# Kernel tuning notes

Measured on AMD Instinct MI355X. Metric: run time of the kernel, lower is better.

The kernel has to match this reference:

```python
import jax, jax.numpy as jnp
import numpy as np

K_CHUNK = 512  # key-chunk size used by the module when n > 5000


def setup_inputs() -> dict:
    key = jax.random.key(0)
    ks = jax.random.split(key, 9)
    b, n, d = 1, 8192, 512
    s = 1.0 / np.sqrt(d)
    x = jax.random.normal(ks[0], (b, n, d), dtype=jnp.float32)
    Wq = jax.random.normal(ks[1], (d, d), dtype=jnp.float32) * s
    bq = jax.random.normal(ks[2], (d,), dtype=jnp.float32) * 0.01
    Wk = jax.random.normal(ks[3], (d, d), dtype=jnp.float32) * s
    bk = jax.random.normal(ks[4], (d,), dtype=jnp.float32) * 0.01
    Wv = jax.random.normal(ks[5], (d, d), dtype=jnp.float32) * s
    bv = jax.random.normal(ks[6], (d,), dtype=jnp.float32) * 0.01
    Wo = jax.random.normal(ks[7], (d, d), dtype=jnp.float32) * s
    bo = jax.random.normal(ks[8], (d,), dtype=jnp.float32) * 0.01
    return {"x": x, "Wq": Wq, "bq": bq, "Wk": Wk, "bk": bk,
            "Wv": Wv, "bv": bv, "Wo": Wo, "bo": bo}


def reference(x, Wq, bq, Wk, bk, Wv, bv, Wo, bo):
    # Faithful to the n > 5000 branch of SimpleAttenLayer (eval mode: dropout = identity).
    # The q-chunking in the original does not change the math (each q row is independent),
    # so we vectorize over all queries. The k-chunking DOES change the math: softmax is
    # applied within each 512-wide key block, then a second softmax over the concatenated
    # per-block weights, then matmul with full v.
    b, n, d = x.shape
    assert n % K_CHUNK == 0
    q = x @ Wq + bq
    k = x @ Wk + bk
    v = x @ Wv + bv
    scores = jnp.einsum('bnd,bmd->bnm', q, k) / jnp.sqrt(jnp.float32(d))
    # softmax within each key chunk of size K_CHUNK
    w1 = jax.nn.softmax(scores.reshape(b, n, n // K_CHUNK, K_CHUNK), axis=-1)
    w1 = w1.reshape(b, n, n)
    # second (global) softmax over the concatenated chunk weights
    w2 = jax.nn.softmax(w1, axis=-1)
    attn_out = jnp.einsum('bnm,bmd->bnd', w2, v)
    cls_attn_weights = w2[:, 0:1, :]  # [b, 1, n]
    out = x + (attn_out @ Wo + bo)
    return (out, cls_attn_weights)
```

## Files before the change

### kernel.cpp

```cpp
#include <hip/hip_runtime.h>
#include <stdint.h>

typedef unsigned short u16;
typedef uint8_t u8;
typedef __bf16 bf16x8 __attribute__((ext_vector_type(8)));
typedef float f32x4 __attribute__((ext_vector_type(4)));
typedef float f32x16 __attribute__((ext_vector_type(16)));
typedef long i64x2 __attribute__((ext_vector_type(2)));
typedef int i32x8 __attribute__((ext_vector_type(8)));

#define NTOK 8192
#define DD 512
#define CHK 512
#define NCH 16
#define KSPLIT 2
#define KLEN 4096
#define LOG2E 1.4426950408889634f
#define SCL 0.044194173824159216f
#define SCLL 0.063762069130835270f

__device__ __forceinline__ u16 f2bf(float f) {
  union { float f; uint32_t u; } v; v.f = f;
  uint32_t r = v.u + 0x7FFFu + ((v.u >> 16) & 1u);
  return (u16)(r >> 16);
}

template <int CTRL>
__device__ __forceinline__ float dppadd(float x) {
  int y = __builtin_amdgcn_update_dpp(0, __float_as_int(x), CTRL, 0xF, 0xF, true);
  return x + __int_as_float(y);
}
__device__ __forceinline__ float rowsum16(float x) {
  x = dppadd<0xB1>(x);
  x = dppadd<0x4E>(x);
  x = dppadd<0x141>(x);
  x = dppadd<0x140>(x);
  return x;
}

typedef const __attribute__((address_space(1))) unsigned int* gas_t;
typedef __attribute__((address_space(3))) unsigned int* las_t;
__device__ __forceinline__ void gload16(const void* g, void* l) {
  __builtin_amdgcn_global_load_lds((gas_t)g, (las_t)l, 16, 0, 0);
}

__device__ __forceinline__ void vm4bar() {
  asm volatile("s_waitcnt vmcnt(4)\n\ts_barrier" ::: "memory");
}
__device__ __forceinline__ void vm0bar() {
  asm volatile("s_waitcnt vmcnt(0)\n\ts_barrier" ::: "memory");
}
__device__ __forceinline__ void barx() {
  asm volatile("s_barrier" ::: "memory");
}
__device__ __forceinline__ void lgkm0() {
  asm volatile("s_waitcnt lgkmcnt(0)" ::: "memory");
  __builtin_amdgcn_sched_barrier(0);
}

__device__ __forceinline__ int ilv64(int p) {
  const int g = p >> 3;
  return (((g & 3) * 2) + (g >> 2)) * 8 + (p & 7);
}

__global__ void prep_kernel(const float* __restrict__ x, const float* __restrict__ Wq,
                            const float* __restrict__ Wk, const float* __restrict__ Wv,
                            const float* __restrict__ Wo, const float* __restrict__ bq,
                            u16* __restrict__ xb, u16* __restrict__ Wall, u16* __restrict__ WoT,
                            float* __restrict__ lsum, float* __restrict__ q0g) {
  __shared__ float t[32][33];
  const int bid = blockIdx.x;
  const int tid = threadIdx.x;
  if (bid < 4096) {
    int i = bid * 256 + tid;
    if (bid < 32) lsum[bid * 256 + tid] = 0.f;
    float4 v = ((const float4*)x)[i];
    ushort4 o;
    o.x = f2bf(v.x); o.y = f2bf(v.y); o.z = f2bf(v.z); o.w = f2bf(v.w);
    ((ushort4*)xb)[i] = o;
  } else if (bid < 5120) {
    const int tt = bid - 4096;
    const int z = tt >> 8, idx = tt & 255;
    const float* W; u16* WT;
    if (z == 0)      { W = Wq; WT = Wall; }
    else if (z == 1) { W = Wk; WT = Wall + 512 * 512; }
    else if (z == 2) { W = Wv; WT = Wall + 2 * 512 * 512; }
    else             { W = Wo; WT = WoT; }
    const int n0 = (idx & 15) * 32, k0 = (idx >> 4) * 32;
    const int tx = tid & 31, ty = tid >> 5;
    #pragma unroll
    for (int i = 0; i < 4; i++)
      t[ty + 8 * i][tx] = W[(k0 + ty + 8 * i) * DD + n0 + tx];
    __syncthreads();
    #pragma unroll
    for (int i = 0; i < 4; i++)
      WT[(n0 + ty + 8 * i) * DD + k0 + tx] = f2bf(t[tx][ty + 8 * i]);
  } else {
    const int c = (bid - 5120) * 256 + tid;
    float acc = bq[c];
    #pragma unroll 8
    for (int i = 0; i < 512; i++) acc += x[i] * Wq[i * 512 + c];
    q0g[c] = acc;
  }
}

__launch_bounds__(256, 3)
__global__ void qkv_kernel(const u16* __restrict__ A, const u16* __restrict__ Wall,
                           const float* __restrict__ bq, const float* __restrict__ bk,
                           const float* __restrict__ bv, u8* __restrict__ qb8,
                           u8* __restrict__ kb8, u8* __restrict__ vT8) {
  __shared__ __align__(16) u16 As[2][128 * 32];
  __shared__ __align__(16) u16 Bs[2][128 * 32];
  const int m0 = blockIdx.x * 128;
  const int n0g = blockIdx.y * 128;
  const int which = blockIdx.y >> 2;
  const int n0 = n0g & 511;
  const int tid = threadIdx.x;
  const int w = tid >> 6, lane = tid & 63, lm = lane & 15, quad = lane >> 4;
  const int wm = w & 1, wn = w >> 1;
  f32x4 acc[4][4] = {};
  const int soff = tid * 16;
  const int srow = soff >> 6;
  const int scol = soff & 63;
  const char* Ag = (const char*)A + ((size_t)(m0 + srow) * DD) * 2 + scol;
  const char* Bg = (const char*)Wall + ((size_t)(n0g + srow) * DD) * 2 + scol;
  char* Al = (char*)As + w * 1024;
  char* Bl = (char*)Bs + w * 1024;
  const size_t rs = (size_t)64 * DD * 2;

  auto stage = [&](int kk, int buf) {
    const char* ag = Ag + (size_t)kk * 2;
    const char* bg = Bg + (size_t)kk * 2;
    char* al = Al + buf * 8192;
    char* bl = Bl + buf * 8192;
    gload16(ag, al);
    gload16(ag + rs, al + 4096);
    gload16(bg, bl);
    gload16(bg + rs, bl + 4096);
  };

  stage(0, 0);
  for (int t = 0; t < 16; ++t) {
    const int cur = t & 1;
    if (t < 15) { stage((t + 1) * 32, cur ^ 1); vm4bar(); }
    else vm0bar();
    bf16x8 af[4], bfr[4];
    #pragma unroll
    for (int i = 0; i < 4; i++) af[i] = *(const bf16x8*)&As[cur][(wm * 64 + i * 16 + lm) * 32 + quad * 8];
    #pragma unroll
    for (int j = 0; j < 4; j++) bfr[j] = *(const bf16x8*)&Bs[cur][(wn * 64 + j * 16 + lm) * 32 + quad * 8];
    lgkm0();
    #pragma unroll
    for (int i = 0; i < 4; i++)
      #pragma unroll
      for (int j = 0; j < 4; j++)
        acc[i][j] = __builtin_amdgcn_mfma_f32_16x16x32_bf16(af[i], bfr[j], acc[i][j], 0, 0, 0);
    barx();
  }
  const float* bias = (which == 0) ? bq : (which == 1) ? bk : bv;
  u8* tile = (u8*)As;
  #pragma unroll
  for (int i = 0; i < 4; i++) {
    const int rl0 = wm * 64 + i * 16 + quad * 4;
    #pragma unroll
    for (int j = 0; j < 4; j++) {
      const int cl = wn * 64 + j * 16 + lm;
      const float bv_ = bias[n0 + cl];
      if (which == 2) {
        #pragma unroll
        for (int r = 0; r < 4; r++) {
          const float val = acc[i][j][r] + bv_;
          uint32_t pk = __builtin_amdgcn_cvt_pk_fp8_f32(val, val, 0, false);
          const int rl = rl0 + r;
          const int t6 = rl & 63;
          const int tl = (rl & 64) | ((t6 & 15) * 4 + (t6 >> 4));
          tile[cl * 128 + tl] = (u8)(pk & 0xFF);
        }
      } else {
        const int icl = (cl & 64) | ilv64(cl & 63);
        #pragma unroll
        for (int r = 0; r < 4; r++) {
          const float val = acc[i][j][r] + bv_;
          uint32_t pk = __builtin_amdgcn_cvt_pk_fp8_f32(val, val, 0, false);
          tile[(rl0 + r) * 128 + icl] = (u8)(pk & 0xFF);
        }
      }
    }
  }
  __syncthreads();
  const int lrow = tid >> 1, half = tid & 1;
  const uint4* s4 = (const uint4*)(tile + lrow * 128 + half * 64);
  if (which == 2) {
    uint4* p = (uint4*)(vT8 + (size_t)(n0 + lrow) * NTOK + m0 + half * 64);
    #pragma unroll
    for (int k = 0; k < 4; k++) p[k] = s4[k];
  } else {
    u8* dst = (which == 0) ? qb8 : kb8;
    uint4* p = (uint4*)(dst + (size_t)(m0 + lrow) * DD + n0 + half * 64);
    #pragma unroll
    for (int k = 0; k < 4; k++) p[k] = s4[k];
  }
}

__launch_bounds__(256, 3)
__global__ void outproj_kernel(const u16* __restrict__ A, const u16* __restrict__ BT,
                               const float* __restrict__ bias, float* __restrict__ outp,
                               const float* __restrict__ resid) {
  __shared__ __align__(16) u16 As[2][128 * 32];
  __shared__ __align__(16) u16 Bs[2][128 * 32];
  const int m0 = blockIdx.x * 128, n0 = blockIdx.y * 128;
  const int tid = threadIdx.x;
  const int w = tid >> 6, lane = tid & 63, lm = lane & 15, quad = lane >> 4;
  const int wm = w & 1, wn = w >> 1;
  f32x4 acc[4][4] = {};
  const int soff = tid * 16;
  const int srow = soff >> 6;
  const int scol = soff & 63;
  const char* Ag = (const char*)A + ((size_t)(m0 + srow) * DD) * 2 + scol;
  const char* Bg = (const char*)BT + ((size_t)(n0 + srow) * DD) * 2 + scol;
  char* Al = (char*)As + w * 1024;
  char* Bl = (char*)Bs + w * 1024;
  const size_t rs = (size_t)64 * DD * 2;

  auto stage = [&](int kk, int buf) {
    const char* ag = Ag + (size_t)kk * 2;
    const char* bg = Bg + (size_t)kk * 2;
    char* al = Al + buf * 8192;
    char* bl = Bl + buf * 8192;
    gload16(ag, al);
    gload16(ag + rs, al + 4096);
    gload16(bg, bl);
    gload16(bg + rs, bl + 4096);
  };

  stage(0, 0);
  for (int t = 0; t < 16; ++t) {
    const int cur = t & 1;
    if (t < 15) { stage((t + 1) * 32, cur ^ 1); vm4bar(); }
    else vm0bar();
    bf16x8 af[4], bfr[4];
    #pragma unroll
    for (int i = 0; i < 4; i++) af[i] = *(const bf16x8*)&As[cur][(wm * 64 + i * 16 + lm) * 32 + quad * 8];
    #pragma unroll
    for (int j = 0; j < 4; j++) bfr[j] = *(const bf16x8*)&Bs[cur][(wn * 64 + j * 16 + lm) * 32 + quad * 8];
    lgkm0();
    #pragma unroll
    for (int i = 0; i < 4; i++)
      #pragma unroll
      for (int j = 0; j < 4; j++)
        acc[i][j] = __builtin_amdgcn_mfma_f32_16x16x32_bf16(af[i], bfr[j], acc[i][j], 0, 0, 0);
    barx();
  }
  #pragma unroll
  for (int i = 0; i < 4; i++) {
    const int row0 = m0 + wm * 64 + i * 16 + quad * 4;
    #pragma unroll
    for (int j = 0; j < 4; j++) {
      const int col = n0 + wn * 64 + j * 16 + lm;
      const float bv = bias[col];
      #pragma unroll
      for (int r = 0; r < 4; r++) {
        const size_t idx = (size_t)(row0 + r) * DD + col;
        outp[idx] = acc[i][j][r] + bv + resid[idx];
      }
    }
  }
}

template <int MODE>
__launch_bounds__(256, 3)
__global__ void gemm_pv_kernel(const u8* __restrict__ A, const u8* __restrict__ BT,
                               int K, void* __restrict__ outp,
                               const float* __restrict__ lsum) {
  __shared__ __align__(16) u8 As[2][128 * 64];
  __shared__ __align__(16) u8 Bs[2][128 * 64];
  const int m0 = blockIdx.x * 128, n0 = blockIdx.y * 128;
  const int tid = threadIdx.x;
  const int w = tid >> 6, lane = tid & 63;
  const int l31 = lane & 31, kh = lane >> 5;
  const int wm = w & 1, wn = w >> 1;
  f32x16 acc[2][2] = {};
  const int srow = tid >> 2;
  const int scol = ((tid & 3) ^ ((srow >> 1) & 3)) * 16;
  const size_t kbase = (size_t)blockIdx.z * (size_t)K;
  const u8* Ag = A + (size_t)(m0 + srow) * NTOK + kbase + scol;
  const u8* Bg = BT + (size_t)(n0 + srow) * NTOK + kbase + scol;
  u8* Al = (u8*)As + w * 1024;
  u8* Bl = (u8*)Bs + w * 1024;
  const size_t rs = (size_t)64 * NTOK;
  const int s_ = (l31 >> 1) & 3;
  const int c0 = ((kh * 2) ^ s_) * 16;
  const int c1 = ((kh * 2 + 1) ^ s_) * 16;

  auto stage = [&](int kk, int buf) {
    gload16(Ag + kk, Al + buf * 8192);
    gload16(Ag + kk + rs, Al + buf * 8192 + 4096);
    gload16(Bg + kk, Bl + buf * 8192);
    gload16(Bg + kk + rs, Bl + buf * 8192 + 4096);
  };

  stage(0, 0);
  int cur = 0;
  for (int kk = 0; kk < K; kk += 64) {
    if (kk + 64 < K) { stage(kk + 64, cur ^ 1); vm4bar(); }
    else vm0bar();
    i32x8 av[2], bv[2];
    #pragma unroll
    for (int g = 0; g < 2; g++) {
      const int ar = wm * 64 + g * 32 + l31;
      union { i32x8 v; struct { i64x2 lo; i64x2 hi; } p; } ua;
      ua.p.lo = *(const i64x2*)&As[cur][ar * 64 + c0];
      ua.p.hi = *(const i64x2*)&As[cur][ar * 64 + c1];
      av[g] = ua.v;
      const int br = wn * 64 + g * 32 + l31;
      union { i32x8 v; struct { i64x2 lo; i64x2 hi; } p; } ub;
      ub.p.lo = *(const i64x2*)&Bs[cur][br * 64 + c0];
      ub.p.hi = *(const i64x2*)&Bs[cur][br * 64 + c1];
      bv[g] = ub.v;
    }
    lgkm0();
    #pragma unroll
    for (int i = 0; i < 2; i++)
      #pragma unroll
      for (int j = 0; j < 2; j++)
        acc[i][j] = __builtin_amdgcn_mfma_scale_f32_32x32x64_f8f6f4(
            av[i], bv[j], acc[i][j], 0, 0, 0, 0x7F7F7F7F, 0, 0x7F7F7F7F);
    barx();
    cur ^= 1;
  }
  #pragma unroll
  for (int i = 0; i < 2; i++) {
    #pragma unroll
    for (int j = 0; j < 2; j++) {
      #pragma unroll
      for (int r = 0; r < 16; r++) {
        const int row = m0 + wm * 64 + i * 32 + (r & 3) + 8 * (r >> 2) + 4 * kh;
        const int col = n0 + wn * 64 + j * 32 + l31;
        if (MODE == 3) {
          ((u16*)outp)[(size_t)row * DD + col] = f2bf(acc[i][j][r] * (1.0f / lsum[row]));
        } else {
          float* po = (float*)outp + (size_t)blockIdx.z * NTOK * DD;
          po[(size_t)row * DD + col] = acc[i][j][r];
        }
      }
    }
  }
}

__global__ void pv_reduce_kernel(const float* __restrict__ part, const float* __restrict__ lsum,
                                 u16* __restrict__ attnb) {
  const int idx = blockIdx.x * 256 + threadIdx.x;
  const int row = idx >> 7;
  const int c4 = (idx & 127) << 2;
  const float* p = part + (size_t)row * DD + c4;
  const size_t stride = (size_t)NTOK * DD;
  float4 a = *(const float4*)(p);
  float4 b = *(const float4*)(p + stride);
  const float inv = 1.0f / lsum[row];
  ushort4 o;
  o.x = f2bf((a.x + b.x) * inv);
  o.y = f2bf((a.y + b.y) * inv);
  o.z = f2bf((a.z + b.z) * inv);
  o.w = f2bf((a.w + b.w) * inv);
  *(ushort4*)(attnb + (size_t)row * DD + c4) = o;
}

__launch_bounds__(512, 4)
__global__ void scores_kernel(const u8* __restrict__ qb8, const u8* __restrict__ kb8,
                              u8* __restrict__ P8, float* __restrict__ lsum) {
  __shared__ __align__(16) u8 As[2][64 * 64];
  __shared__ __align__(16) u8 Bs[2][512 * 64];
  __shared__ float hS[8][64], hP[8][64], hZ[64];
  const int m0 = blockIdx.x * 64;
  const int c = blockIdx.y;
  const int tid = threadIdx.x;
  const int w = tid >> 6, lane = tid & 63, lm = lane & 15, quad = lane >> 4;
  const int wsl = w;
  f32x4 s[4][4] = {};
  const int srA = tid >> 2;
  const int scS = ((tid & 3) ^ ((srA >> 1) & 3)) * 16;
  const u8* Qg = qb8 + (size_t)(m0 + srA) * DD + scS;
  const u8* Kg = kb8 + (size_t)(c * CHK + srA) * DD + scS;
  u8* Al = (u8*)As + w * 1024;
  u8* Bl = (u8*)Bs + w * 1024;
  const int csel = ((quad ^ ((lm >> 1) & 3)) * 16);

  auto stage = [&](int kk, int buf) {
    u8* al = Al + buf * 4096;
    u8* bl = Bl + buf * 32768;
    if (tid < 256) gload16(Qg + kk, al);
    gload16(Kg + kk, bl);
    gload16(Kg + kk + (size_t)128 * DD, bl + 8192);
    gload16(Kg + kk + (size_t)256 * DD, bl + 16384);
    gload16(Kg + kk + (size_t)384 * DD, bl + 24576);
  };

  stage(0, 0);
  vm0bar();
  #pragma unroll
  for (int t = 0; t < 8; ++t) {
    const int cur = t & 1;
    if (t < 7) stage((t + 1) * 64, cur ^ 1);
    i64x2 afv[4], bfv[4];
    #pragma unroll
    for (int i = 0; i < 4; i++)
      afv[i] = *(const i64x2*)&As[cur][(i * 16 + lm) * 64 + csel];
    #pragma unroll
    for (int j = 0; j < 4; j++)
      bfv[j] = *(const i64x2*)&Bs[cur][(wsl * 64 + j * 16 + lm) * 64 + csel];
    lgkm0();
    __builtin_amdgcn_s_setprio(1);
    #pragma unroll
    for (int i = 0; i < 4; i++)
      #pragma unroll
      for (int j = 0; j < 4; j++) {
        s[i][j] = __builtin_amdgcn_mfma_f32_16x16x32_fp8_fp8(afv[i].x, bfv[j].x, s[i][j], 0, 0, 0);
        s[i][j] = __builtin_amdgcn_mfma_f32_16x16x32_fp8_fp8(afv[i].y, bfv[j].y, s[i][j], 0, 0, 0);
      }
    __builtin_amdgcn_s_setprio(0);
    vm0bar();
  }
  #pragma unroll
  for (int i = 0; i < 4; i++) {
    #pragma unroll
    for (int reg = 0; reg < 4; reg++) {
      float z = 0.f;
      #pragma unroll
      for (int j = 0; j < 4; j++) {
        float e = exp2f(s[i][j][reg] * SCLL);
        s[i][j][reg] = e;
        z += e;
      }
      z = rowsum16(z);
      if (lm == 0) hS[wsl][i * 16 + quad * 4 + reg] = z;
    }
  }
  __syncthreads();
  if (tid < 64) {
    float t = 0.f;
    #pragma unroll
    for (int w2 = 0; w2 < 8; w2++) t += hS[w2][tid];
    hZ[tid] = LOG2E / t;
  }
  __syncthreads();
  const int pbyte = wsl * 64 + lm * 4;
  #pragma unroll
  for (int i = 0; i < 4; i++) {
    #pragma unroll
    for (int reg = 0; reg < 4; reg++) {
      const int rl = i * 16 + quad * 4 + reg;
      const float iz = hZ[rl];
      const float p0 = exp2f(s[i][0][reg] * iz);
      const float p1 = exp2f(s[i][1][reg] * iz);
      const float p2 = exp2f(s[i][2][reg] * iz);
      const float p3 = exp2f(s[i][3][reg] * iz);
      float zp = (p0 + p1) + (p2 + p3);
      zp = rowsum16(zp);
      if (lm == 0) hP[wsl][rl] = zp;
      uint32_t o = __builtin_amdgcn_cvt_pk_fp8_f32(p0, p1, 0, false);
      o = __builtin_amdgcn_cvt_pk_fp8_f32(p2, p3, o, true);
      *(uint32_t*)(P8 + (size_t)(m0 + rl) * NTOK + c * CHK + pbyte) = o;
    }
  }
  __syncthreads();
  if (tid < 64) {
    float t = 0.f;
    #pragma unroll
    for (int w2 = 0; w2 < 8; w2++) t += hP[w2][tid];
    atomicAdd(&lsum[m0 + tid], t);
  }
}

__global__ void cls_u_kernel(const float* __restrict__ Wk, const float* __restrict__ bk,
                             const float* __restrict__ q0g, float* __restrict__ uc) {
  __shared__ float q0[512];
  const int tid = threadIdx.x;
  q0[tid] = q0g[tid];
  q0[tid + 256] = q0g[tid + 256];
  __syncthreads();
  if (blockIdx.x < 8) {
    const int c = blockIdx.x * 64 + (tid >> 2), ii = tid & 3;
    float acc = 0.f;
    #pragma unroll 8
    for (int j = ii; j < 512; j += 4) acc += Wk[(size_t)c * 512 + j] * q0[j];
    acc += __shfl_xor(acc, 1, 64);
    acc += __shfl_xor(acc, 2, 64);
    if (ii == 0) uc[c] = acc;
  } else if (tid < 64) {
    float acc = 0.f;
    #pragma unroll 8
    for (int j = tid; j < 512; j += 64) acc += bk[j] * q0[j];
    #pragma unroll
    for (int off = 1; off < 64; off <<= 1) acc += __shfl_xor(acc, off, 64);
    if (tid == 0) uc[512] = acc;
  }
}

__global__ void cls_scores_kernel(const float* __restrict__ x, const float* __restrict__ uc,
                                  float* __restrict__ s0) {
  __shared__ float u[512];
  __shared__ float c0s;
  int tid = threadIdx.x;
  for (int i = tid; i < 512; i += 256) u[i] = uc[i];
  if (tid == 0) c0s = uc[512];
  __syncthreads();
  int rowg = blockIdx.x * 32 + (tid >> 3);
  int ii = tid & 7;
  const float* xr = x + rowg * 512;
  float acc = 0.f;
  for (int i = ii; i < 512; i += 8) acc += xr[i] * u[i];
  acc += __shfl_xor(acc, 1, 64);
  acc += __shfl_xor(acc, 2, 64);
  acc += __shfl_xor(acc, 4, 64);
  if (ii == 0) s0[rowg] = (acc + c0s) * SCL;
}

__global__ void cls_softmax_kernel(const float* __restrict__ s0, float* __restrict__ out) {
  int tid = threadIdx.x;
  int w = tid >> 6, lane = tid & 63;
  const float* sc = s0 + w * 512;
  float v[8];
  float m = -1e30f;
  #pragma unroll
  for (int j = 0; j < 8; j++) { v[j] = sc[lane * 8 + j]; m = fmaxf(m, v[j]); }
  for (int off = 1; off < 64; off <<= 1) m = fmaxf(m, __shfl_xor(m, off, 64));
  float z = 0.f;
  #pragma unroll
  for (int j = 0; j < 8; j++) { v[j] = expf(v[j] - m); z += v[j]; }
  for (int off = 1; off < 64; off <<= 1) z += __shfl_xor(z, off, 64);
  float invz = 1.f / z;
  float l = 0.f;
  #pragma unroll
  for (int j = 0; j < 8; j++) { v[j] = expf(v[j] * invz); l += v[j]; }
  for (int off = 1; off < 64; off <<= 1) l += __shfl_xor(l, off, 64);
  __shared__ float lw[16];
  if (lane == 0) lw[w] = l;
  __syncthreads();
  float L = 0.f;
  for (int i = 0; i < 16; i++) L += lw[i];
  float invL = 1.f / L;
  #pragma unroll
  for (int j = 0; j < 8; j++) out[w * 512 + lane * 8 + j] = v[j] * invL;
}

extern "C" void kernel_launch(void* const* d_in, const int* in_sizes, int n_in,
                              void* d_out, int out_size, void* d_ws, size_t ws_size,
                              hipStream_t stream) {
  const float* x  = (const float*)d_in[0];
  const float* Wq = (const float*)d_in[1];
  const float* bq = (const float*)d_in[2];
  const float* Wk = (const float*)d_in[3];
  const float* bk = (const float*)d_in[4];
  const float* Wv = (const float*)d_in[5];
  const float* bv = (const float*)d_in[6];
  const float* Wo = (const float*)d_in[7];
  const float* bo = (const float*)d_in[8];
  float* out = (float*)d_out;

  char* ws = (char*)d_ws;
  u16* xb    = (u16*)(ws);
  u16* Wall  = (u16*)(ws + 8388608);
  u16* WoT   = (u16*)(ws + 9961472);
  u8*  qb8   = (u8*)(ws + 10485760);
  u8*  kb8   = (u8*)(ws + 14680064);
  u8*  vT8   = (u8*)(ws + 18874368);
  u16* attnb = (u16*)(ws + 23068672);
  float* q0g = (float*)(ws + 31457280);
  float* uc  = (float*)(ws + 31461376);
  float* s0  = (float*)(ws + 31465472);
  float* lsum= (float*)(ws + 31498240);
  u8*  P8    = (u8*)(ws + 31531008);
  float* part= (float*)(ws + 98639872);
  const size_t need_full = 98639872ULL + (size_t)KSPLIT * NTOK * DD * 4ULL;

  prep_kernel<<<5122, 256, 0, stream>>>(x, Wq, Wk, Wv, Wo, bq, xb, Wall, WoT, lsum, q0g);

  qkv_kernel<<<dim3(NTOK / 128, 12), 256, 0, stream>>>(xb, Wall, bq, bk, bv, qb8, kb8, vT8);

  scores_kernel<<<dim3(NTOK / 64, NCH), 512, 0, stream>>>(qb8, kb8, P8, lsum);

  if (ws_size >= need_full) {
    gemm_pv_kernel<4><<<dim3(NTOK / 128, DD / 128, KSPLIT), 256, 0, stream>>>(
        P8, vT8, KLEN, part, nullptr);
    pv_reduce_kernel<<<NTOK * DD / 4 / 256, 256, 0, stream>>>(part, lsum, attnb);
  } else {
    gemm_pv_kernel<3><<<dim3(NTOK / 128, DD / 128), 256, 0, stream>>>(
        P8, vT8, NTOK, attnb, lsum);
  }

  outproj_kernel<<<dim3(NTOK / 128, DD / 128), 256, 0, stream>>>(attnb, WoT, bo, out, x);

  cls_u_kernel<<<9, 256, 0, stream>>>(Wk, bk, q0g, uc);
  cls_scores_kernel<<<NTOK / 32, 256, 0, stream>>>(x, uc, s0);
  cls_softmax_kernel<<<1, 1024, 0, stream>>>(s0, out + (size_t)NTOK * DD);
}
```

Measured before the change: 300.4 us.

## Fold CLS-row kernels into qkv and outproj launches with ticket-based final softmax

The three small CLS-attention kernels are removed. The u-vector computation becomes an extra grid row of the QKV GEMM launch, and the per-row CLS scores become extra blocks of the output-projection launch. An atomic ticket, reset in the prep kernel, lets the last finishing block run the CLS double softmax. This removes three kernel launches and their serialization tails, at the cost of threadfence/atomic synchronization and extra non-GEMM blocks sharing the GEMM grids.

```diff
diff --git a/kernel.cpp b/kernel.cpp
--- a/kernel.cpp
+++ b/kernel.cpp
@@ -67,13 +67,15 @@
                             const float* __restrict__ Wk, const float* __restrict__ Wv,
                             const float* __restrict__ Wo, const float* __restrict__ bq,
                             u16* __restrict__ xb, u16* __restrict__ Wall, u16* __restrict__ WoT,
-                            float* __restrict__ lsum, float* __restrict__ q0g) {
+                            float* __restrict__ lsum, float* __restrict__ q0g,
+                            unsigned int* __restrict__ ticket) {
   __shared__ float t[32][33];
   const int bid = blockIdx.x;
   const int tid = threadIdx.x;
   if (bid < 4096) {
     int i = bid * 256 + tid;
     if (bid < 32) lsum[bid * 256 + tid] = 0.f;
+    if (bid == 0 && tid == 0) *ticket = 0u;
     float4 v = ((const float4*)x)[i];
     ushort4 o;
     o.x = f2bf(v.x); o.y = f2bf(v.y); o.z = f2bf(v.z); o.w = f2bf(v.w);
@@ -108,14 +110,40 @@
 __global__ void qkv_kernel(const u16* __restrict__ A, const u16* __restrict__ Wall,
                            const float* __restrict__ bq, const float* __restrict__ bk,
                            const float* __restrict__ bv, u8* __restrict__ qb8,
-                           u8* __restrict__ kb8, u8* __restrict__ vT8) {
+                           u8* __restrict__ kb8, u8* __restrict__ vT8,
+                           const float* __restrict__ WkF, const float* __restrict__ bkF,
+                           const float* __restrict__ q0g, float* __restrict__ uc) {
   __shared__ __align__(16) u16 As[2][128 * 32];
   __shared__ __align__(16) u16 Bs[2][128 * 32];
+  const int tid = threadIdx.x;
+  if (blockIdx.y == 12) {
+    if (blockIdx.x >= 9) return;
+    float* q0 = (float*)As;
+    q0[tid] = q0g[tid];
+    q0[tid + 256] = q0g[tid + 256];
+    __syncthreads();
+    if (blockIdx.x < 8) {
+      const int c = blockIdx.x * 64 + (tid >> 2), ii = tid & 3;
+      float acc = 0.f;
+      #pragma unroll 8
+      for (int j = ii; j < 512; j += 4) acc += WkF[(size_t)c * 512 + j] * q0[j];
+      acc += __shfl_xor(acc, 1, 64);
+      acc += __shfl_xor(acc, 2, 64);
+      if (ii == 0) uc[c] = acc;
+    } else if (tid < 64) {
+      float acc = 0.f;
+      #pragma unroll 8
+      for (int j = tid; j < 512; j += 64) acc += bkF[j] * q0[j];
+      #pragma unroll
+      for (int off = 1; off < 64; off <<= 1) acc += __shfl_xor(acc, off, 64);
+      if (tid == 0) uc[512] = acc;
+    }
+    return;
+  }
   const int m0 = blockIdx.x * 128;
   const int n0g = blockIdx.y * 128;
   const int which = blockIdx.y >> 2;
   const int n0 = n0g & 511;
-  const int tid = threadIdx.x;
   const int w = tid >> 6, lane = tid & 63, lm = lane & 15, quad = lane >> 4;
   const int wm = w & 1, wn = w >> 1;
   f32x4 acc[4][4] = {};
@@ -205,11 +233,71 @@
 __launch_bounds__(256, 3)
 __global__ void outproj_kernel(const u16* __restrict__ A, const u16* __restrict__ BT,
                                const float* __restrict__ bias, float* __restrict__ outp,
-                               const float* __restrict__ resid) {
+                               const float* __restrict__ resid, const float* __restrict__ uc,
+                               float* __restrict__ s0, unsigned int* __restrict__ ticket) {
   __shared__ __align__(16) u16 As[2][128 * 32];
   __shared__ __align__(16) u16 Bs[2][128 * 32];
+  const int tid = threadIdx.x;
+  if (blockIdx.y >= 4) {
+    const int cb = (blockIdx.y - 4) * 64 + blockIdx.x;
+    __shared__ float u[512];
+    __shared__ float c0s;
+    __shared__ int sOld;
+    for (int i = tid; i < 512; i += 256) u[i] = uc[i];
+    if (tid == 0) c0s = uc[512];
+    __syncthreads();
+    const int rowg = cb * 32 + (tid >> 3);
+    const int ii = tid & 7;
+    const float* xr = resid + (size_t)rowg * 512;
+    float a2 = 0.f;
+    for (int i = ii; i < 512; i += 8) a2 += xr[i] * u[i];
+    a2 += __shfl_xor(a2, 1, 64);
+    a2 += __shfl_xor(a2, 2, 64);
+    a2 += __shfl_xor(a2, 4, 64);
+    if (ii == 0) s0[rowg] = (a2 + c0s) * SCL;
+    __threadfence();
+    __syncthreads();
+    if (tid == 0) sOld = (int)atomicAdd(ticket, 1u);
+    __syncthreads();
+    if (sOld == 255) {
+      __threadfence();
+      __shared__ float lw2[16];
+      const int wv = tid >> 6, lane = tid & 63;
+      float vv[4][8];
+      #pragma unroll
+      for (int cc = 0; cc < 4; cc++) {
+        const int ch = wv * 4 + cc;
+        const float* sc = s0 + ch * 512;
+        float m = -1e30f;
+        #pragma unroll
+        for (int j = 0; j < 8; j++) { vv[cc][j] = sc[lane * 8 + j]; m = fmaxf(m, vv[cc][j]); }
+        for (int off = 1; off < 64; off <<= 1) m = fmaxf(m, __shfl_xor(m, off, 64));
+        float z = 0.f;
+        #pragma unroll
+        for (int j = 0; j < 8; j++) { vv[cc][j] = expf(vv[cc][j] - m); z += vv[cc][j]; }
+        for (int off = 1; off < 64; off <<= 1) z += __shfl_xor(z, off, 64);
+        const float invz = 1.f / z;
+        float l = 0.f;
+        #pragma unroll
+        for (int j = 0; j < 8; j++) { vv[cc][j] = expf(vv[cc][j] * invz); l += vv[cc][j]; }
+        for (int off = 1; off < 64; off <<= 1) l += __shfl_xor(l, off, 64);
+        if (lane == 0) lw2[ch] = l;
+      }
+      __syncthreads();
+      float L = 0.f;
+      #pragma unroll
+      for (int i = 0; i < 16; i++) L += lw2[i];
+      const float invL = 1.f / L;
+      float* outc = outp + (size_t)NTOK * DD;
+      #pragma unroll
+      for (int cc = 0; cc < 4; cc++)
+        #pragma unroll
+        for (int j = 0; j < 8; j++)
+          outc[(wv * 4 + cc) * 512 + lane * 8 + j] = vv[cc][j] * invL;
+    }
+    return;
+  }
   const int m0 = blockIdx.x * 128, n0 = blockIdx.y * 128;
-  const int tid = threadIdx.x;
   const int w = tid >> 6, lane = tid & 63, lm = lane & 15, quad = lane >> 4;
   const int wm = w & 1, wn = w >> 1;
   f32x4 acc[4][4] = {};
@@ -471,78 +559,6 @@
   }
 }
 
-__global__ void cls_u_kernel(const float* __restrict__ Wk, const float* __restrict__ bk,
-                             const float* __restrict__ q0g, float* __restrict__ uc) {
-  __shared__ float q0[512];
-  const int tid = threadIdx.x;
-  q0[tid] = q0g[tid];
-  q0[tid + 256] = q0g[tid + 256];
-  __syncthreads();
-  if (blockIdx.x < 8) {
-    const int c = blockIdx.x * 64 + (tid >> 2), ii = tid & 3;
-    float acc = 0.f;
-    #pragma unroll 8
-    for (int j = ii; j < 512; j += 4) acc += Wk[(size_t)c * 512 + j] * q0[j];
-    acc += __shfl_xor(acc, 1, 64);
-    acc += __shfl_xor(acc, 2, 64);
-    if (ii == 0) uc[c] = acc;
-  } else if (tid < 64) {
-    float acc = 0.f;
-    #pragma unroll 8
-    for (int j = tid; j < 512; j += 64) acc += bk[j] * q0[j];
-    #pragma unroll
-    for (int off = 1; off < 64; off <<= 1) acc += __shfl_xor(acc, off, 64);
-    if (tid == 0) uc[512] = acc;
-  }
-}
-
-__global__ void cls_scores_kernel(const float* __restrict__ x, const float* __restrict__ uc,
-                                  float* __restrict__ s0) {
-  __shared__ float u[512];
-  __shared__ float c0s;
-  int tid = threadIdx.x;
-  for (int i = tid; i < 512; i += 256) u[i] = uc[i];
-  if (tid == 0) c0s = uc[512];
-  __syncthreads();
-  int rowg = blockIdx.x * 32 + (tid >> 3);
-  int ii = tid & 7;
-  const float* xr = x + rowg * 512;
-  float acc = 0.f;
-  for (int i = ii; i < 512; i += 8) acc += xr[i] * u[i];
-  acc += __shfl_xor(acc, 1, 64);
-  acc += __shfl_xor(acc, 2, 64);
-  acc += __shfl_xor(acc, 4, 64);
-  if (ii == 0) s0[rowg] = (acc + c0s) * SCL;
-}
-
-__global__ void cls_softmax_kernel(const float* __restrict__ s0, float* __restrict__ out) {
-  int tid = threadIdx.x;
-  int w = tid >> 6, lane = tid & 63;
-  const float* sc = s0 + w * 512;
-  float v[8];
-  float m = -1e30f;
-  #pragma unroll
-  for (int j = 0; j < 8; j++) { v[j] = sc[lane * 8 + j]; m = fmaxf(m, v[j]); }
-  for (int off = 1; off < 64; off <<= 1) m = fmaxf(m, __shfl_xor(m, off, 64));
-  float z = 0.f;
-  #pragma unroll
-  for (int j = 0; j < 8; j++) { v[j] = expf(v[j] - m); z += v[j]; }
-  for (int off = 1; off < 64; off <<= 1) z += __shfl_xor(z, off, 64);
-  float invz = 1.f / z;
-  float l = 0.f;
-  #pragma unroll
-  for (int j = 0; j < 8; j++) { v[j] = expf(v[j] * invz); l += v[j]; }
-  for (int off = 1; off < 64; off <<= 1) l += __shfl_xor(l, off, 64);
-  __shared__ float lw[16];
-  if (lane == 0) lw[w] = l;
-  __syncthreads();
-  float L = 0.f;
-  for (int i = 0; i < 16; i++) L += lw[i];
-  float invL = 1.f / L;
-  #pragma unroll
-  for (int j = 0; j < 8; j++) out[w * 512 + lane * 8 + j] = v[j] * invL;
-}
-
 extern "C" void kernel_launch(void* const* d_in, const int* in_sizes, int n_in,
                               void* d_out, int out_size, void* d_ws, size_t ws_size,
                               hipStream_t stream) {
@@ -566,6 +582,7 @@
   u8*  vT8   = (u8*)(ws + 18874368);
   u16* attnb = (u16*)(ws + 23068672);
   float* q0g = (float*)(ws + 31457280);
+  unsigned int* ticket = (unsigned int*)(ws + 31460352);
   float* uc  = (float*)(ws + 31461376);
   float* s0  = (float*)(ws + 31465472);
   float* lsum= (float*)(ws + 31498240);
@@ -573,9 +590,10 @@
   float* part= (float*)(ws + 98639872);
   const size_t need_full = 98639872ULL + (size_t)KSPLIT * NTOK * DD * 4ULL;
 
-  prep_kernel<<<5122, 256, 0, stream>>>(x, Wq, Wk, Wv, Wo, bq, xb, Wall, WoT, lsum, q0g);
-
-  qkv_kernel<<<dim3(NTOK / 128, 12), 256, 0, stream>>>(xb, Wall, bq, bk, bv, qb8, kb8, vT8);
+  prep_kernel<<<5122, 256, 0, stream>>>(x, Wq, Wk, Wv, Wo, bq, xb, Wall, WoT, lsum, q0g, ticket);
+
+  qkv_kernel<<<dim3(NTOK / 128, 13), 256, 0, stream>>>(xb, Wall, bq, bk, bv, qb8, kb8, vT8,
+                                                       Wk, bk, q0g, uc);
 
   scores_kernel<<<dim3(NTOK / 64, NCH), 512, 0, stream>>>(qb8, kb8, P8, lsum);
 
@@ -588,9 +606,5 @@
         P8, vT8, NTOK, attnb, lsum);
   }
 
-  outproj_kernel<<<dim3(NTOK / 128, DD / 128), 256, 0, stream>>>(attnb, WoT, bo, out, x);
-
-  cls_u_kernel<<<9, 256, 0, stream>>>(Wk, bk, q0g, uc);
-  cls_scores_kernel<<<NTOK / 32, 256, 0, stream>>>(x, uc, s0);
-  cls_softmax_kernel<<<1, 1024, 0, stream>>>(s0, out + (size_t)NTOK * DD);
-}
+  outproj_kernel<<<dim3(NTOK / 128, 8), 256, 0, stream>>>(attnb, WoT, bo, out, x, uc, s0, ticket);
+}
```

After: 306.5 us. +2.1%, slower.
